# Optimization experiments

Hardware: AMD Instinct MI355X
Metric: run time of the kernel (lower is better)

Reference implementation:

```python
import math
import jax, jax.numpy as jnp
import numpy as np

FILTER_ORDER = 64
FILTER_EMB_DIM = 5
HIDDEN = 256
SHIFT = 0.05
FAST_DECAY_PCT = 0.3
SLOW_DECAY_PCT = 1.5
TARGET = 0.01


def setup_inputs() -> dict:
    key = jax.random.key(0)
    ks = jax.random.split(key, 8)
    B, C, L = 8, HIDDEN, 8192

    def lin_w(k, fan_out, fan_in):
        return jax.random.normal(k, (fan_out, fan_in), jnp.float32) / np.sqrt(fan_in).astype(np.float32)

    return {
        "x": jax.random.normal(ks[0], (B, C, L), jnp.float32),
        "W1": lin_w(ks[1], FILTER_ORDER, FILTER_EMB_DIM),
        "b1": jnp.zeros((FILTER_ORDER,), jnp.float32),
        "freq0": jnp.ones((1, FILTER_ORDER), jnp.float32),
        "W2": lin_w(ks[2], FILTER_ORDER, FILTER_ORDER),
        "b2": jnp.zeros((FILTER_ORDER,), jnp.float32),
        "freq1": jnp.ones((1, FILTER_ORDER), jnp.float32),
        "W3": lin_w(ks[3], FILTER_ORDER, FILTER_ORDER),
        "b3": jnp.zeros((FILTER_ORDER,), jnp.float32),
        "freq2": jnp.ones((1, FILTER_ORDER), jnp.float32),
        "Wout": lin_w(ks[4], HIDDEN, FILTER_ORDER),
        "D": jax.random.normal(ks[5], (HIDDEN,), jnp.float32),
        "L": L,
    }


def _pos_emb(L):
    # HyenaDnaPositionalEmbedding: z (1, L, emb_dim), t (1, L, 1)
    t = jnp.linspace(0.0, 1.0, L, dtype=jnp.float32)[None, :, None]
    t_rescaled = jnp.linspace(0.0, L - 1, L, dtype=jnp.float32)[None, :, None]
    w = 2.0 * math.pi * t_rescaled / L  # (1, L, 1)
    bands = (FILTER_EMB_DIM - 1) // 2
    f = jnp.linspace(1e-4, bands - 1, bands, dtype=jnp.float32)[None, None]  # (1, 1, bands)
    z = jnp.concatenate([t, jnp.cos(-f * w), jnp.sin(-f * w)], axis=-1)  # (1, L, emb_dim)
    return z, t


def _filter_kernel(W1, b1, freq0, W2, b2, freq1, W3, b3, freq2, Wout, L):
    z, t = _pos_emb(L)
    h = jnp.sin(freq0 * (jnp.einsum('ble,oe->blo', z, W1) + b1))
    h = jnp.sin(freq1 * (jnp.einsum('blo,po->blp', h, W2) + b2))
    h = jnp.sin(freq2 * (jnp.einsum('blo,po->blp', h, W3) + b3))
    h = jnp.einsum('blo,do->bld', h, Wout)  # (1, L, HIDDEN)
    # exponential modulation window
    max_decay = math.log(TARGET) / FAST_DECAY_PCT
    min_decay = math.log(TARGET) / SLOW_DECAY_PCT
    deltas = jnp.linspace(min_decay, max_decay, HIDDEN, dtype=jnp.float32)[None, None]
    decay = jnp.exp(-t * jnp.abs(deltas))  # (1, L, HIDDEN)
    h = h * (decay + SHIFT)
    return h[0].T  # (HIDDEN, L) channels-major kernel


def _fftconv(u, k, D):
    # y = conv(u, k) + u * D via FFT, zero-padded to 2L (linear convolution)
    L = u.shape[-1]
    fft_size = 2 * L
    k_f = jnp.fft.rfft(k.astype(jnp.float32), n=fft_size) / fft_size  # (C, fft_size//2+1)
    u_f = jnp.fft.rfft(u.astype(jnp.float32), n=fft_size)             # (B, C, fft_size//2+1)
    y = jnp.fft.irfft(u_f * k_f, n=fft_size, norm='forward')[..., :L]
    return (y + u * D[:, None]).astype(u.dtype)


def reference(x, W1, b1, freq0, W2, b2, freq1, W3, b3, freq2, Wout, D, L):
    k = _filter_kernel(W1, b1, freq0, W2, b2, freq1, W3, b3, freq2, Wout, L)
    return _fftconv(x, k, D)
```

## Files before the change

kernel.cpp:

```cpp
#include <hip/hip_runtime.h>

#define L_SEQ 8192
#define NTH 512
#define HID 256
#define PIDX(i) ((i) + ((i) >> 5))
#define LDS_SZ 8448

#define ANG16 3.83495196971410315e-4f
#define ANG8  7.66990393942820630e-4f

__device__ __forceinline__ float2 cmul(float2 a, float2 b) {
  return make_float2(a.x*b.x - a.y*b.y, a.x*b.y + a.y*b.x);
}
__device__ __forceinline__ float2 cadd(float2 a, float2 b){ return make_float2(a.x+b.x, a.y+b.y); }
__device__ __forceinline__ float2 csub(float2 a, float2 b){ return make_float2(a.x-b.x, a.y-b.y); }

__device__ __forceinline__ void bf4_fwd(float2 a0, float2 a1, float2 a2, float2 a3,
                                        float2& o0, float2& o1, float2& o2, float2& o3) {
  float2 t0 = cadd(a0,a2), t1 = csub(a0,a2), t2 = cadd(a1,a3), t3 = csub(a1,a3);
  o0 = cadd(t0,t2);
  o2 = csub(t0,t2);
  o1 = make_float2(t1.x + t3.y, t1.y - t3.x);
  o3 = make_float2(t1.x - t3.y, t1.y + t3.x);
}
__device__ __forceinline__ void bf4_inv(float2 c0, float2 c1, float2 c2, float2 c3,
                                        float2& o0, float2& o1, float2& o2, float2& o3) {
  float2 u0 = cadd(c0,c2), u2 = csub(c0,c2), u1 = cadd(c1,c3);
  float2 v3 = make_float2(c3.y - c1.y, c1.x - c3.x);
  o0 = cadd(u0,u1); o2 = csub(u0,u1); o1 = cadd(u2,v3); o3 = csub(u2,v3);
}

__device__ __constant__ const float W16C[4] = {1.0f, 0.92387953251128674f, 0.70710678118654752f, 0.38268343236508977f};
__device__ __constant__ const float W16S[4] = {0.0f, -0.38268343236508977f, -0.70710678118654752f, -0.92387953251128674f};
__device__ __constant__ const float C16[10] = {1.0f, 0.92387953251128674f, 0.70710678118654752f, 0.38268343236508977f,
                                               0.0f, -0.38268343236508977f, -0.70710678118654752f, -0.92387953251128674f,
                                               -1.0f, -0.92387953251128674f};
__device__ __constant__ const float S16[10] = {0.0f, -0.38268343236508977f, -0.70710678118654752f, -0.92387953251128674f,
                                               -1.0f, -0.92387953251128674f, -0.70710678118654752f, -0.38268343236508977f,
                                               0.0f, 0.38268343236508977f};

template<int MB>
__device__ __forceinline__ void fwd_pair(float2* __restrict__ X, int tid) {
  const int MQ = MB / 4;
  int g = tid / MQ;
  int i2 = tid - g*MQ;
  int base = g*4*MB + i2;
  float2 e[4][4];
  #pragma unroll
  for (int a = 0; a < 4; ++a)
    #pragma unroll
    for (int b = 0; b < 4; ++b)
      e[a][b] = X[PIDX(base + a*MQ + b*MB)];
  float sb, cb;
  __sincosf(-6.2831853071795864769f * (float)i2 / (float)(4*MB), &sb, &cb);
  float2 wb = make_float2(cb, sb);
  float2 f[4][4];
  #pragma unroll
  for (int a = 0; a < 4; ++a) {
    float2 wa = cmul(wb, make_float2(W16C[a], W16S[a]));
    float2 w2 = cmul(wa, wa), w3 = cmul(w2, wa);
    float2 o0,o1,o2,o3;
    bf4_fwd(e[a][0], e[a][1], e[a][2], e[a][3], o0,o1,o2,o3);
    f[a][0] = o0; f[a][1] = cmul(o1,wa); f[a][2] = cmul(o2,w2); f[a][3] = cmul(o3,w3);
  }
  float2 wp = cmul(wb,wb); wp = cmul(wp,wp);
  float2 wp2 = cmul(wp,wp), wp3 = cmul(wp2,wp);
  #pragma unroll
  for (int b = 0; b < 4; ++b) {
    float2 o0,o1,o2,o3;
    bf4_fwd(f[0][b], f[1][b], f[2][b], f[3][b], o0,o1,o2,o3);
    X[PIDX(base + 0*MQ + b*MB)] = o0;
    X[PIDX(base + 1*MQ + b*MB)] = cmul(o1,wp);
    X[PIDX(base + 2*MQ + b*MB)] = cmul(o2,wp2);
    X[PIDX(base + 3*MQ + b*MB)] = cmul(o3,wp3);
  }
}

template<int MB>
__device__ __forceinline__ void inv_pair(float2* __restrict__ X, int tid) {
  const int MQ = MB / 4;
  int g = tid / MQ;
  int i2 = tid - g*MQ;
  int base = g*4*MB + i2;
  float2 e[4][4];
  #pragma unroll
  for (int a = 0; a < 4; ++a)
    #pragma unroll
    for (int b = 0; b < 4; ++b)
      e[a][b] = X[PIDX(base + a*MQ + b*MB)];
  float sb, cb;
  __sincosf(6.2831853071795864769f * (float)i2 / (float)(4*MB), &sb, &cb);
  float2 wb = make_float2(cb, sb);
  float2 wq = cmul(wb,wb); wq = cmul(wq,wq);
  float2 wq2 = cmul(wq,wq), wq3 = cmul(wq2,wq);
  float2 f[4][4];
  #pragma unroll
  for (int b = 0; b < 4; ++b) {
    float2 c0 = e[0][b];
    float2 c1 = cmul(e[1][b], wq);
    float2 c2 = cmul(e[2][b], wq2);
    float2 c3 = cmul(e[3][b], wq3);
    float2 o0,o1,o2,o3;
    bf4_inv(c0,c1,c2,c3, o0,o1,o2,o3);
    f[0][b]=o0; f[1][b]=o1; f[2][b]=o2; f[3][b]=o3;
  }
  #pragma unroll
  for (int a = 0; a < 4; ++a) {
    float2 W1 = cmul(wb, make_float2(W16C[a], -W16S[a]));
    float2 W2 = cmul(W1,W1), W3 = cmul(W2,W1);
    float2 c0 = f[a][0];
    float2 c1 = cmul(f[a][1], W1);
    float2 c2 = cmul(f[a][2], W2);
    float2 c3 = cmul(f[a][3], W3);
    float2 o0,o1,o2,o3;
    bf4_inv(c0,c1,c2,c3, o0,o1,o2,o3);
    X[PIDX(base + a*MQ + 0*MB)] = o0;
    X[PIDX(base + a*MQ + 1*MB)] = o1;
    X[PIDX(base + a*MQ + 2*MB)] = o2;
    X[PIDX(base + a*MQ + 3*MB)] = o3;
  }
}

__device__ __forceinline__ void fwd41(float2 P[16]) {
  #pragma unroll
  for (int i = 0; i < 4; ++i) {
    float2 o0,o1,o2,o3;
    bf4_fwd(P[i], P[i+4], P[i+8], P[i+12], o0,o1,o2,o3);
    P[i]    = o0;
    P[i+4]  = cmul(o1, make_float2(C16[i],   S16[i]));
    P[i+8]  = cmul(o2, make_float2(C16[2*i], S16[2*i]));
    P[i+12] = cmul(o3, make_float2(C16[3*i], S16[3*i]));
  }
  #pragma unroll
  for (int q = 0; q < 4; ++q) {
    float2 o0,o1,o2,o3;
    bf4_fwd(P[4*q],P[4*q+1],P[4*q+2],P[4*q+3], o0,o1,o2,o3);
    P[4*q]=o0; P[4*q+1]=o1; P[4*q+2]=o2; P[4*q+3]=o3;
  }
}
__device__ __forceinline__ void inv14(float2 P[16]) {
  #pragma unroll
  for (int q = 0; q < 4; ++q) {
    float2 o0,o1,o2,o3;
    bf4_inv(P[4*q],P[4*q+1],P[4*q+2],P[4*q+3], o0,o1,o2,o3);
    P[4*q]=o0; P[4*q+1]=o1; P[4*q+2]=o2; P[4*q+3]=o3;
  }
  #pragma unroll
  for (int i = 0; i < 4; ++i) {
    float2 c0 = P[i];
    float2 c1 = cmul(P[i+4],  make_float2(C16[i],   -S16[i]));
    float2 c2 = cmul(P[i+8],  make_float2(C16[2*i], -S16[2*i]));
    float2 c3 = cmul(P[i+12], make_float2(C16[3*i], -S16[3*i]));
    float2 o0,o1,o2,o3;
    bf4_inv(c0,c1,c2,c3, o0,o1,o2,o3);
    P[i]=o0; P[i+4]=o1; P[i+8]=o2; P[i+12]=o3;
  }
}

__global__ __launch_bounds__(256) void mlp_kernel(
    const float* __restrict__ W1, const float* __restrict__ b1, const float* __restrict__ fq0,
    const float* __restrict__ W2, const float* __restrict__ b2, const float* __restrict__ fq1,
    const float* __restrict__ W3, const float* __restrict__ b3, const float* __restrict__ fq2,
    float* __restrict__ h3g) {
  __shared__ float hs[2][16][64];
  int tid = threadIdx.x;
  int lane = tid & 63, w = tid >> 6;
  int l0 = blockIdx.x * 16;

  float w1r[5];
  #pragma unroll
  for (int e = 0; e < 5; ++e) w1r[e] = W1[lane*5+e];
  float b1v = b1[lane], f0 = fq0[lane];
  #pragma unroll
  for (int r = 0; r < 4; ++r) {
    int l = l0 + w + 4*r;
    float t = (float)l * (1.0f / (float)(L_SEQ - 1));
    float ang = 6.2831853071795864769f * (float)l / (float)L_SEQ;
    float s0, c0, s1, c1;
    __sincosf(1e-4f * ang, &s0, &c0);
    __sincosf(ang, &s1, &c1);
    float acc = b1v + t*w1r[0] + c0*w1r[1] + c1*w1r[2] - s0*w1r[3] - s1*w1r[4];
    hs[0][w + 4*r][lane] = __sinf(f0 * acc);
  }
  __syncthreads();

  float wr[64];
  #pragma unroll
  for (int j = 0; j < 16; ++j) *(float4*)&wr[4*j] = *(const float4*)&W2[lane*64 + 4*j];
  float b2v = b2[lane], f1 = fq1[lane];
  #pragma unroll
  for (int r = 0; r < 4; ++r) {
    int ll = w + 4*r;
    float a0 = 0.f, a1 = 0.f, a2 = 0.f, a3 = 0.f;
    #pragma unroll
    for (int o = 0; o < 64; o += 4) {
      a0 += hs[0][ll][o+0] * wr[o+0];
      a1 += hs[0][ll][o+1] * wr[o+1];
      a2 += hs[0][ll][o+2] * wr[o+2];
      a3 += hs[0][ll][o+3] * wr[o+3];
    }
    hs[1][ll][lane] = __sinf(f1 * (b2v + ((a0+a1)+(a2+a3))));
  }
  __syncthreads();

  #pragma unroll
  for (int j = 0; j < 16; ++j) *(float4*)&wr[4*j] = *(const float4*)&W3[lane*64 + 4*j];
  float b3v = b3[lane], f2 = fq2[lane];
  #pragma unroll
  for (int r = 0; r < 4; ++r) {
    int ll = w + 4*r;
    float a0 = 0.f, a1 = 0.f, a2 = 0.f, a3 = 0.f;
    #pragma unroll
    for (int o = 0; o < 64; o += 4) {
      a0 += hs[1][ll][o+0] * wr[o+0];
      a1 += hs[1][ll][o+1] * wr[o+1];
      a2 += hs[1][ll][o+2] * wr[o+2];
      a3 += hs[1][ll][o+3] * wr[o+3];
    }
    h3g[(size_t)(l0 + ll) * 64 + lane] = __sinf(f2 * (b3v + ((a0+a1)+(a2+a3))));
  }
}

__global__ __launch_bounds__(256) void kwrite_kernel(const float* __restrict__ h3g,
                                                     const float* __restrict__ Wout,
                                                     const float* __restrict__ Dv,
                                                     float* __restrict__ kbuf) {
  __shared__ float tileh[256][65];
  int tid = threadIdx.x;
  int l0 = blockIdx.x * 256;
  int c0 = blockIdx.y * 32;
  {
    const float4* src = (const float4*)(h3g + (size_t)l0 * 64);
    #pragma unroll
    for (int q = 0; q < 16; ++q) {
      int idx = tid + 256*q;
      int row = idx >> 4, col4 = idx & 15;
      float4 v = src[idx];
      tileh[row][col4*4+0] = v.x;
      tileh[row][col4*4+1] = v.y;
      tileh[row][col4*4+2] = v.z;
      tileh[row][col4*4+3] = v.w;
    }
  }
  __syncthreads();
  float hr[64];
  #pragma unroll
  for (int o = 0; o < 64; ++o) hr[o] = tileh[tid][o];
  int l = l0 + tid;
  float t = (float)l * (1.0f / (float)(L_SEQ - 1));
  const float mind = -3.0701134573253945f;
  const float maxd = -15.350567286626972f;
  for (int jj = 0; jj < 32; ++jj) {
    int c = c0 + jj;
    float a0 = 0.f, a1 = 0.f, a2 = 0.f, a3 = 0.f;
    #pragma unroll
    for (int o = 0; o < 64; o += 4) {
      a0 += hr[o+0] * Wout[c*64+o+0];
      a1 += hr[o+1] * Wout[c*64+o+1];
      a2 += hr[o+2] * Wout[c*64+o+2];
      a3 += hr[o+3] * Wout[c*64+o+3];
    }
    float acc = (a0+a1)+(a2+a3);
    float delta = mind + (maxd - mind) * ((float)c * (1.0f/255.0f));
    float dec = __expf(-t * fabsf(delta)) + 0.05f;
    float v = acc * dec;
    if (l == 0) v += Dv[c];
    kbuf[(size_t)c * L_SEQ + l] = v;
  }
}

__global__ __launch_bounds__(NTH) void kf_kernel(const float* __restrict__ kbuf,
                                                 float2* __restrict__ Kf) {
  __shared__ float2 X[LDS_SZ];
  int c = blockIdx.x;
  int pipe = blockIdx.y;
  int tid = threadIdx.x;
  const float* kr = kbuf + (size_t)c * L_SEQ;
  const float sc = 1.0f / 16384.0f;

  #pragma unroll
  for (int r = 0; r < 2; ++r) {
    int n = 4*tid + 2048*r;
    float4 lo = *(const float4*)(kr + n);
    float4 hi = *(const float4*)(kr + n + 4096);
    #pragma unroll
    for (int j = 0; j < 4; ++j) {
      float klo = ((const float*)&lo)[j];
      float khi = ((const float*)&hi)[j];
      float2 vlo, vhi, w8;
      if (pipe == 0) {
        float sn, cn; __sincosf(-ANG8 * (float)(n+j), &sn, &cn);
        vlo = make_float2(klo, 0.f);
        vhi = make_float2(khi, 0.f);
        w8 = make_float2(cn, sn);
      } else {
        float sn, cn; __sincosf(-ANG16 * (float)(n+j), &sn, &cn);
        vlo = make_float2(klo*cn, klo*sn);
        vhi = make_float2(khi*sn, -khi*cn);
        w8 = cmul(make_float2(cn, sn), make_float2(cn, sn));
      }
      X[PIDX(n+j)]        = cadd(vlo, vhi);
      X[PIDX(n+j+4096)]   = cmul(csub(vlo, vhi), w8);
    }
  }
  __syncthreads();
  fwd_pair<1024>(X, tid); __syncthreads();
  fwd_pair<64>(X, tid);   __syncthreads();
  {
    float2 P[16];
    int base = tid*16;
    #pragma unroll
    for (int j = 0; j < 16; ++j) P[j] = X[PIDX(base+j)];
    fwd41(P);
    float2* out = Kf + (size_t)c * 16384 + pipe*8192 + base;
    #pragma unroll
    for (int j = 0; j < 16; ++j) out[j] = make_float2(P[j].x*sc, P[j].y*sc);
  }
}

template<int PIPE>
__global__ __launch_bounds__(NTH) void conv_pipe(const float* __restrict__ x,
                                                 const float2* __restrict__ Kf,
                                                 float* __restrict__ y) {
  __shared__ float2 X[LDS_SZ];
  int c = blockIdx.x;
  int p = blockIdx.y;
  int tid = threadIdx.x;
  const float* u0 = x + ((size_t)p       * HID + c) * L_SEQ;
  const float* u1 = x + ((size_t)(p + 4) * HID + c) * L_SEQ;
  const float2* K = Kf + (size_t)c * 16384 + PIPE*8192;
  float* y0 = y + ((size_t)p       * HID + c) * L_SEQ;
  float* y1 = y + ((size_t)(p + 4) * HID + c) * L_SEQ;

  #pragma unroll
  for (int r = 0; r < 2; ++r) {
    int n = 4*tid + 2048*r;
    float4 a0 = *(const float4*)(u0 + n);
    float4 a1 = *(const float4*)(u1 + n);
    float4 b0 = *(const float4*)(u0 + n + 4096);
    float4 b1 = *(const float4*)(u1 + n + 4096);
    #pragma unroll
    for (int j = 0; j < 4; ++j) {
      float2 vlo, vhi, w8;
      if (PIPE == 0) {
        float sn, cn; __sincosf(-ANG8 * (float)(n+j), &sn, &cn);
        vlo = make_float2(((const float*)&a0)[j], ((const float*)&a1)[j]);
        vhi = make_float2(((const float*)&b0)[j], ((const float*)&b1)[j]);
        w8 = make_float2(cn, sn);
      } else {
        float sn, cn; __sincosf(-ANG16 * (float)(n+j), &sn, &cn);
        float2 w16 = make_float2(cn, sn);
        vlo = cmul(make_float2(((const float*)&a0)[j], ((const float*)&a1)[j]), w16);
        vhi = cmul(make_float2(((const float*)&b0)[j], ((const float*)&b1)[j]),
                   make_float2(sn, -cn));
        w8 = cmul(w16, w16);
      }
      X[PIDX(n+j)]      = cadd(vlo, vhi);
      X[PIDX(n+j+4096)] = cmul(csub(vlo, vhi), w8);
    }
  }
  __syncthreads();
  fwd_pair<1024>(X, tid); __syncthreads();
  fwd_pair<64>(X, tid);   __syncthreads();
  {
    float2 P[16];
    int base = tid*16;
    #pragma unroll
    for (int j = 0; j < 16; ++j) P[j] = X[PIDX(base+j)];
    fwd41(P);
    #pragma unroll
    for (int j = 0; j < 16; ++j) P[j] = cmul(P[j], K[base+j]);
    inv14(P);
    #pragma unroll
    for (int j = 0; j < 16; ++j) X[PIDX(base+j)] = P[j];
  }
  __syncthreads();
  inv_pair<64>(X, tid);   __syncthreads();
  inv_pair<1024>(X, tid); __syncthreads();
  #pragma unroll
  for (int r = 0; r < 2; ++r) {
    int n = 4*tid + 2048*r;
    float4 w00, w01, w10, w11;
    #pragma unroll
    for (int j = 0; j < 4; ++j) {
      float2 P = X[PIDX(n+j)], Q = X[PIDX(n+j+4096)];
      float2 lo, hi;
      if (PIPE == 1) {
        float sn, cn; __sincosf(ANG16 * (float)(n+j), &sn, &cn);
        float2 w16b = make_float2(cn, sn);
        float2 w8b = cmul(w16b, w16b);
        float2 t = cmul(Q, w8b);
        lo = cmul(cadd(P, t), w16b);
        hi = cmul(csub(P, t), make_float2(-w16b.y, w16b.x));
      } else {
        float sn, cn; __sincosf(ANG8 * (float)(n+j), &sn, &cn);
        float2 t = cmul(Q, make_float2(cn, sn));
        lo = cadd(P, t);
        hi = csub(P, t);
      }
      ((float*)&w00)[j] = lo.x; ((float*)&w01)[j] = lo.y;
      ((float*)&w10)[j] = hi.x; ((float*)&w11)[j] = hi.y;
    }
    if (PIPE == 0) {
      float4 p00 = *(const float4*)(y0 + n);
      float4 p01 = *(const float4*)(y1 + n);
      float4 p10 = *(const float4*)(y0 + n + 4096);
      float4 p11 = *(const float4*)(y1 + n + 4096);
      w00.x += p00.x; w00.y += p00.y; w00.z += p00.z; w00.w += p00.w;
      w01.x += p01.x; w01.y += p01.y; w01.z += p01.z; w01.w += p01.w;
      w10.x += p10.x; w10.y += p10.y; w10.z += p10.z; w10.w += p10.w;
      w11.x += p11.x; w11.y += p11.y; w11.z += p11.z; w11.w += p11.w;
    }
    *(float4*)(y0 + n)        = w00;
    *(float4*)(y1 + n)        = w01;
    *(float4*)(y0 + n + 4096) = w10;
    *(float4*)(y1 + n + 4096) = w11;
  }
}

extern "C" void kernel_launch(void* const* d_in, const int* in_sizes, int n_in,
                              void* d_out, int out_size, void* d_ws, size_t ws_size,
                              hipStream_t stream) {
  const float* x    = (const float*)d_in[0];
  const float* W1   = (const float*)d_in[1];
  const float* b1   = (const float*)d_in[2];
  const float* fq0  = (const float*)d_in[3];
  const float* W2   = (const float*)d_in[4];
  const float* b2   = (const float*)d_in[5];
  const float* fq1  = (const float*)d_in[6];
  const float* W3   = (const float*)d_in[7];
  const float* b3   = (const float*)d_in[8];
  const float* fq2  = (const float*)d_in[9];
  const float* Wout = (const float*)d_in[10];
  const float* Dv   = (const float*)d_in[11];

  float*  kbuf = (float*)d_ws;
  float2* Kf   = (float2*)((char*)d_ws + (size_t)HID * L_SEQ * sizeof(float));
  float*  h3g  = (float*)((char*)d_ws + 38ull*1024*1024);
  float*  y    = (float*)d_out;

  mlp_kernel   <<<dim3(512),    256, 0, stream>>>(W1,b1,fq0,W2,b2,fq1,W3,b3,fq2,h3g);
  kwrite_kernel<<<dim3(32, 8),  256, 0, stream>>>(h3g, Wout, Dv, kbuf);
  kf_kernel    <<<dim3(256,2),  NTH, 0, stream>>>(kbuf, Kf);
  conv_pipe<1> <<<dim3(256,4),  NTH, 0, stream>>>(x, Kf, y);
  conv_pipe<0> <<<dim3(256,4),  NTH, 0, stream>>>(x, Kf, y);
}
```

Baseline: 172.6 us.

## Fuse both conv pipes into one kernel using radix-8 FFT with 1024 threads

The two conv_pipe launches (odd and even half-spectrum) become a single kernel. It loads x once, runs both FFT pipes in sequence, and stashes the first pipe's result in registers, so y no longer has to be written and read back. The FFT moves from radix-4 pairs to radix-8 stages with 1024 threads per block and a new LDS padding. Per-element sincos calls are replaced by incremental twiddle rotation. The exchange is a heavier block with more registers and more barriers, and some precision drift from the recurrent twiddles.

```diff
diff --git a/kernel.cpp b/kernel.cpp
--- a/kernel.cpp
+++ b/kernel.cpp
@@ -1,13 +1,17 @@
 #include <hip/hip_runtime.h>
 
 #define L_SEQ 8192
-#define NTH 512
 #define HID 256
-#define PIDX(i) ((i) + ((i) >> 5))
-#define LDS_SZ 8448
+#define PIDX(i) ((i) + ((i) >> 4))
+#define LDS_SZ 8704
 
 #define ANG16 3.83495196971410315e-4f
 #define ANG8  7.66990393942820630e-4f
+#define CS16 0.99999992646571789f
+#define SN16 3.83495187571395563e-4f
+#define CS8  0.99999970586287223f
+#define SN8  7.66990318742704490e-4f
+#define C707 0.70710678118654752f
 
 __device__ __forceinline__ float2 cmul(float2 a, float2 b) {
   return make_float2(a.x*b.x - a.y*b.y, a.x*b.y + a.y*b.x);
@@ -30,131 +34,106 @@
   o0 = cadd(u0,u1); o2 = csub(u0,u1); o1 = cadd(u2,v3); o3 = csub(u2,v3);
 }
 
-__device__ __constant__ const float W16C[4] = {1.0f, 0.92387953251128674f, 0.70710678118654752f, 0.38268343236508977f};
-__device__ __constant__ const float W16S[4] = {0.0f, -0.38268343236508977f, -0.70710678118654752f, -0.92387953251128674f};
-__device__ __constant__ const float C16[10] = {1.0f, 0.92387953251128674f, 0.70710678118654752f, 0.38268343236508977f,
-                                               0.0f, -0.38268343236508977f, -0.70710678118654752f, -0.92387953251128674f,
-                                               -1.0f, -0.92387953251128674f};
-__device__ __constant__ const float S16[10] = {0.0f, -0.38268343236508977f, -0.70710678118654752f, -0.92387953251128674f,
-                                               -1.0f, -0.92387953251128674f, -0.70710678118654752f, -0.38268343236508977f,
-                                               0.0f, 0.38268343236508977f};
-
-template<int MB>
-__device__ __forceinline__ void fwd_pair(float2* __restrict__ X, int tid) {
-  const int MQ = MB / 4;
-  int g = tid / MQ;
-  int i2 = tid - g*MQ;
-  int base = g*4*MB + i2;
-  float2 e[4][4];
-  #pragma unroll
-  for (int a = 0; a < 4; ++a)
-    #pragma unroll
-    for (int b = 0; b < 4; ++b)
-      e[a][b] = X[PIDX(base + a*MQ + b*MB)];
+__device__ __forceinline__ void fwd8(float2 P[8]) {
+  float2 e0=cadd(P[0],P[4]), e1=cadd(P[1],P[5]), e2=cadd(P[2],P[6]), e3=cadd(P[3],P[7]);
+  float2 o0=csub(P[0],P[4]), o1=csub(P[1],P[5]), o2=csub(P[2],P[6]), o3=csub(P[3],P[7]);
+  o1 = make_float2((o1.x+o1.y)*C707, (o1.y-o1.x)*C707);
+  o2 = make_float2(o2.y, -o2.x);
+  o3 = make_float2((o3.y-o3.x)*C707, -(o3.x+o3.y)*C707);
+  float2 q0,q1,q2,q3;
+  bf4_fwd(e0,e1,e2,e3,q0,q1,q2,q3);
+  P[0]=q0; P[2]=q1; P[4]=q2; P[6]=q3;
+  bf4_fwd(o0,o1,o2,o3,q0,q1,q2,q3);
+  P[1]=q0; P[3]=q1; P[5]=q2; P[7]=q3;
+}
+__device__ __forceinline__ void inv8(float2 P[8]) {
+  float2 E0,E1,E2,E3,O0,O1,O2,O3;
+  bf4_inv(P[0],P[2],P[4],P[6],E0,E1,E2,E3);
+  bf4_inv(P[1],P[3],P[5],P[7],O0,O1,O2,O3);
+  O1 = make_float2((O1.x-O1.y)*C707, (O1.x+O1.y)*C707);
+  O2 = make_float2(-O2.y, O2.x);
+  O3 = make_float2(-(O3.x+O3.y)*C707, (O3.x-O3.y)*C707);
+  P[0]=cadd(E0,O0); P[4]=csub(E0,O0);
+  P[1]=cadd(E1,O1); P[5]=csub(E1,O1);
+  P[2]=cadd(E2,O2); P[6]=csub(E2,O2);
+  P[3]=cadd(E3,O3); P[7]=csub(E3,O3);
+}
+
+template<int M>
+__device__ __forceinline__ void fwd_stage8(float2* __restrict__ X, int t) {
+  int i2 = t & (M-1);
+  int g  = t / M;
+  int base = g*8*M + i2;
+  float2 P[8];
+  #pragma unroll
+  for (int j=0;j<8;++j) P[j] = X[PIDX(base + j*M)];
+  fwd8(P);
   float sb, cb;
-  __sincosf(-6.2831853071795864769f * (float)i2 / (float)(4*MB), &sb, &cb);
-  float2 wb = make_float2(cb, sb);
-  float2 f[4][4];
-  #pragma unroll
-  for (int a = 0; a < 4; ++a) {
-    float2 wa = cmul(wb, make_float2(W16C[a], W16S[a]));
-    float2 w2 = cmul(wa, wa), w3 = cmul(w2, wa);
-    float2 o0,o1,o2,o3;
-    bf4_fwd(e[a][0], e[a][1], e[a][2], e[a][3], o0,o1,o2,o3);
-    f[a][0] = o0; f[a][1] = cmul(o1,wa); f[a][2] = cmul(o2,w2); f[a][3] = cmul(o3,w3);
-  }
-  float2 wp = cmul(wb,wb); wp = cmul(wp,wp);
-  float2 wp2 = cmul(wp,wp), wp3 = cmul(wp2,wp);
-  #pragma unroll
-  for (int b = 0; b < 4; ++b) {
-    float2 o0,o1,o2,o3;
-    bf4_fwd(f[0][b], f[1][b], f[2][b], f[3][b], o0,o1,o2,o3);
-    X[PIDX(base + 0*MQ + b*MB)] = o0;
-    X[PIDX(base + 1*MQ + b*MB)] = cmul(o1,wp);
-    X[PIDX(base + 2*MQ + b*MB)] = cmul(o2,wp2);
-    X[PIDX(base + 3*MQ + b*MB)] = cmul(o3,wp3);
-  }
-}
-
-template<int MB>
-__device__ __forceinline__ void inv_pair(float2* __restrict__ X, int tid) {
-  const int MQ = MB / 4;
-  int g = tid / MQ;
-  int i2 = tid - g*MQ;
-  int base = g*4*MB + i2;
-  float2 e[4][4];
-  #pragma unroll
-  for (int a = 0; a < 4; ++a)
-    #pragma unroll
-    for (int b = 0; b < 4; ++b)
-      e[a][b] = X[PIDX(base + a*MQ + b*MB)];
+  __sincosf(-6.2831853071795864769f * (float)i2 / (float)(8*M), &sb, &cb);
+  float2 w1 = make_float2(cb, sb);
+  float2 w2 = cmul(w1,w1), w3 = cmul(w2,w1), w4 = cmul(w2,w2);
+  float2 w5 = cmul(w4,w1), w6 = cmul(w4,w2), w7 = cmul(w4,w3);
+  X[PIDX(base)]     = P[0];
+  X[PIDX(base+M)]   = cmul(P[1],w1);
+  X[PIDX(base+2*M)] = cmul(P[2],w2);
+  X[PIDX(base+3*M)] = cmul(P[3],w3);
+  X[PIDX(base+4*M)] = cmul(P[4],w4);
+  X[PIDX(base+5*M)] = cmul(P[5],w5);
+  X[PIDX(base+6*M)] = cmul(P[6],w6);
+  X[PIDX(base+7*M)] = cmul(P[7],w7);
+}
+template<int M>
+__device__ __forceinline__ void inv_stage8(float2* __restrict__ X, int t) {
+  int i2 = t & (M-1);
+  int g  = t / M;
+  int base = g*8*M + i2;
   float sb, cb;
-  __sincosf(6.2831853071795864769f * (float)i2 / (float)(4*MB), &sb, &cb);
-  float2 wb = make_float2(cb, sb);
-  float2 wq = cmul(wb,wb); wq = cmul(wq,wq);
-  float2 wq2 = cmul(wq,wq), wq3 = cmul(wq2,wq);
-  float2 f[4][4];
-  #pragma unroll
-  for (int b = 0; b < 4; ++b) {
-    float2 c0 = e[0][b];
-    float2 c1 = cmul(e[1][b], wq);
-    float2 c2 = cmul(e[2][b], wq2);
-    float2 c3 = cmul(e[3][b], wq3);
-    float2 o0,o1,o2,o3;
-    bf4_inv(c0,c1,c2,c3, o0,o1,o2,o3);
-    f[0][b]=o0; f[1][b]=o1; f[2][b]=o2; f[3][b]=o3;
-  }
-  #pragma unroll
-  for (int a = 0; a < 4; ++a) {
-    float2 W1 = cmul(wb, make_float2(W16C[a], -W16S[a]));
-    float2 W2 = cmul(W1,W1), W3 = cmul(W2,W1);
-    float2 c0 = f[a][0];
-    float2 c1 = cmul(f[a][1], W1);
-    float2 c2 = cmul(f[a][2], W2);
-    float2 c3 = cmul(f[a][3], W3);
-    float2 o0,o1,o2,o3;
-    bf4_inv(c0,c1,c2,c3, o0,o1,o2,o3);
-    X[PIDX(base + a*MQ + 0*MB)] = o0;
-    X[PIDX(base + a*MQ + 1*MB)] = o1;
-    X[PIDX(base + a*MQ + 2*MB)] = o2;
-    X[PIDX(base + a*MQ + 3*MB)] = o3;
-  }
-}
-
-__device__ __forceinline__ void fwd41(float2 P[16]) {
-  #pragma unroll
-  for (int i = 0; i < 4; ++i) {
-    float2 o0,o1,o2,o3;
-    bf4_fwd(P[i], P[i+4], P[i+8], P[i+12], o0,o1,o2,o3);
-    P[i]    = o0;
-    P[i+4]  = cmul(o1, make_float2(C16[i],   S16[i]));
-    P[i+8]  = cmul(o2, make_float2(C16[2*i], S16[2*i]));
-    P[i+12] = cmul(o3, make_float2(C16[3*i], S16[3*i]));
-  }
-  #pragma unroll
-  for (int q = 0; q < 4; ++q) {
-    float2 o0,o1,o2,o3;
-    bf4_fwd(P[4*q],P[4*q+1],P[4*q+2],P[4*q+3], o0,o1,o2,o3);
-    P[4*q]=o0; P[4*q+1]=o1; P[4*q+2]=o2; P[4*q+3]=o3;
-  }
-}
-__device__ __forceinline__ void inv14(float2 P[16]) {
-  #pragma unroll
-  for (int q = 0; q < 4; ++q) {
-    float2 o0,o1,o2,o3;
-    bf4_inv(P[4*q],P[4*q+1],P[4*q+2],P[4*q+3], o0,o1,o2,o3);
-    P[4*q]=o0; P[4*q+1]=o1; P[4*q+2]=o2; P[4*q+3]=o3;
-  }
-  #pragma unroll
-  for (int i = 0; i < 4; ++i) {
-    float2 c0 = P[i];
-    float2 c1 = cmul(P[i+4],  make_float2(C16[i],   -S16[i]));
-    float2 c2 = cmul(P[i+8],  make_float2(C16[2*i], -S16[2*i]));
-    float2 c3 = cmul(P[i+12], make_float2(C16[3*i], -S16[3*i]));
-    float2 o0,o1,o2,o3;
-    bf4_inv(c0,c1,c2,c3, o0,o1,o2,o3);
-    P[i]=o0; P[i+4]=o1; P[i+8]=o2; P[i+12]=o3;
-  }
+  __sincosf(6.2831853071795864769f * (float)i2 / (float)(8*M), &sb, &cb);
+  float2 w1 = make_float2(cb, sb);
+  float2 w2 = cmul(w1,w1), w3 = cmul(w2,w1), w4 = cmul(w2,w2);
+  float2 w5 = cmul(w4,w1), w6 = cmul(w4,w2), w7 = cmul(w4,w3);
+  float2 P[8];
+  P[0] = X[PIDX(base)];
+  P[1] = cmul(X[PIDX(base+M)],  w1);
+  P[2] = cmul(X[PIDX(base+2*M)],w2);
+  P[3] = cmul(X[PIDX(base+3*M)],w3);
+  P[4] = cmul(X[PIDX(base+4*M)],w4);
+  P[5] = cmul(X[PIDX(base+5*M)],w5);
+  P[6] = cmul(X[PIDX(base+6*M)],w6);
+  P[7] = cmul(X[PIDX(base+7*M)],w7);
+  inv8(P);
+  #pragma unroll
+  for (int j=0;j<8;++j) X[PIDX(base + j*M)] = P[j];
+}
+
+__device__ __forceinline__ void fft_mid_fwd(float2* __restrict__ X, int t) {
+  __syncthreads();
+  fwd_stage8<512>(X,t); __syncthreads();
+  fwd_stage8<64>(X,t);  __syncthreads();
+  fwd_stage8<8>(X,t);   __syncthreads();
+}
+__device__ __forceinline__ void fft_mid_inv(float2* __restrict__ X, int t) {
+  __syncthreads();
+  inv_stage8<8>(X,t);   __syncthreads();
+  inv_stage8<64>(X,t);  __syncthreads();
+  inv_stage8<512>(X,t); __syncthreads();
+}
+
+__device__ __forceinline__ void middle_pointwise(float2* __restrict__ X,
+                                                 const float2* __restrict__ K, int t) {
+  int base = 8*t;
+  float2 kreg[8];
+  #pragma unroll
+  for (int r=0;r<8;++r) kreg[r] = K[base+r];
+  float2 P[8];
+  #pragma unroll
+  for (int r=0;r<8;++r) P[r] = X[PIDX(base+r)];
+  fwd8(P);
+  #pragma unroll
+  for (int r=0;r<8;++r) P[r] = cmul(P[r], kreg[r]);
+  inv8(P);
+  #pragma unroll
+  for (int r=0;r<8;++r) X[PIDX(base+r)] = P[r];
 }
 
 __global__ __launch_bounds__(256) void mlp_kernel(
@@ -269,152 +248,141 @@
   }
 }
 
-__global__ __launch_bounds__(NTH) void kf_kernel(const float* __restrict__ kbuf,
-                                                 float2* __restrict__ Kf) {
+__global__ __launch_bounds__(1024) void kf_kernel(const float* __restrict__ kbuf,
+                                                  float2* __restrict__ Kf) {
   __shared__ float2 X[LDS_SZ];
-  int c = blockIdx.x;
-  int pipe = blockIdx.y;
-  int tid = threadIdx.x;
+  int pipe = blockIdx.x;
+  int c = blockIdx.y;
+  int t = threadIdx.x;
   const float* kr = kbuf + (size_t)c * L_SEQ;
   const float sc = 1.0f / 16384.0f;
-
-  #pragma unroll
-  for (int r = 0; r < 2; ++r) {
-    int n = 4*tid + 2048*r;
-    float4 lo = *(const float4*)(kr + n);
-    float4 hi = *(const float4*)(kr + n + 4096);
-    #pragma unroll
-    for (int j = 0; j < 4; ++j) {
-      float klo = ((const float*)&lo)[j];
-      float khi = ((const float*)&hi)[j];
-      float2 vlo, vhi, w8;
-      if (pipe == 0) {
-        float sn, cn; __sincosf(-ANG8 * (float)(n+j), &sn, &cn);
-        vlo = make_float2(klo, 0.f);
-        vhi = make_float2(khi, 0.f);
-        w8 = make_float2(cn, sn);
-      } else {
-        float sn, cn; __sincosf(-ANG16 * (float)(n+j), &sn, &cn);
-        vlo = make_float2(klo*cn, klo*sn);
-        vhi = make_float2(khi*sn, -khi*cn);
-        w8 = cmul(make_float2(cn, sn), make_float2(cn, sn));
-      }
-      X[PIDX(n+j)]        = cadd(vlo, vhi);
-      X[PIDX(n+j+4096)]   = cmul(csub(vlo, vhi), w8);
-    }
-  }
-  __syncthreads();
-  fwd_pair<1024>(X, tid); __syncthreads();
-  fwd_pair<64>(X, tid);   __syncthreads();
-  {
-    float2 P[16];
-    int base = tid*16;
-    #pragma unroll
-    for (int j = 0; j < 16; ++j) P[j] = X[PIDX(base+j)];
-    fwd41(P);
-    float2* out = Kf + (size_t)c * 16384 + pipe*8192 + base;
-    #pragma unroll
-    for (int j = 0; j < 16; ++j) out[j] = make_float2(P[j].x*sc, P[j].y*sc);
-  }
-}
-
-template<int PIPE>
-__global__ __launch_bounds__(NTH) void conv_pipe(const float* __restrict__ x,
-                                                 const float2* __restrict__ Kf,
-                                                 float* __restrict__ y) {
+  int n0 = 4*t;
+  float4 lo4 = *(const float4*)(kr + n0);
+  float4 hi4 = *(const float4*)(kr + n0 + 4096);
+  if (pipe == 0) {
+    float sb, cb; __sincosf(-ANG8 * (float)n0, &sb, &cb);
+    float2 w8 = make_float2(cb, sb);
+    #pragma unroll
+    for (int j = 0; j < 4; ++j) {
+      if (j) w8 = cmul(w8, make_float2(CS8, -SN8));
+      float klo = ((const float*)&lo4)[j];
+      float khi = ((const float*)&hi4)[j];
+      X[PIDX(n0+j)]      = make_float2(klo + khi, 0.f);
+      float d = klo - khi;
+      X[PIDX(n0+j+4096)] = make_float2(d * w8.x, d * w8.y);
+    }
+  } else {
+    float sb, cb; __sincosf(-ANG16 * (float)n0, &sb, &cb);
+    float2 w16 = make_float2(cb, sb);
+    #pragma unroll
+    for (int j = 0; j < 4; ++j) {
+      if (j) w16 = cmul(w16, make_float2(CS16, -SN16));
+      float klo = ((const float*)&lo4)[j];
+      float khi = ((const float*)&hi4)[j];
+      float2 vlo = make_float2(klo * w16.x, klo * w16.y);
+      float2 vhi = make_float2(khi * w16.y, -khi * w16.x);
+      float2 w8 = cmul(w16, w16);
+      X[PIDX(n0+j)]      = cadd(vlo, vhi);
+      X[PIDX(n0+j+4096)] = cmul(csub(vlo, vhi), w8);
+    }
+  }
+  fft_mid_fwd(X, t);
+  int base = 8*t;
+  float2 P[8];
+  #pragma unroll
+  for (int r=0;r<8;++r) P[r] = X[PIDX(base+r)];
+  fwd8(P);
+  float2* out = Kf + (size_t)c * 16384 + pipe*8192 + base;
+  #pragma unroll
+  for (int r=0;r<8;++r) out[r] = make_float2(P[r].x*sc, P[r].y*sc);
+}
+
+__global__ __launch_bounds__(1024) void conv_kernel(const float* __restrict__ x,
+                                                    const float2* __restrict__ Kf,
+                                                    float* __restrict__ y) {
   __shared__ float2 X[LDS_SZ];
-  int c = blockIdx.x;
-  int p = blockIdx.y;
-  int tid = threadIdx.x;
+  int p = blockIdx.x;
+  int c = blockIdx.y;
+  int t = threadIdx.x;
   const float* u0 = x + ((size_t)p       * HID + c) * L_SEQ;
   const float* u1 = x + ((size_t)(p + 4) * HID + c) * L_SEQ;
-  const float2* K = Kf + (size_t)c * 16384 + PIPE*8192;
+  const float2* KA = Kf + (size_t)c * 16384;
+  const float2* KB = KA + 8192;
   float* y0 = y + ((size_t)p       * HID + c) * L_SEQ;
   float* y1 = y + ((size_t)(p + 4) * HID + c) * L_SEQ;
 
-  #pragma unroll
-  for (int r = 0; r < 2; ++r) {
-    int n = 4*tid + 2048*r;
-    float4 a0 = *(const float4*)(u0 + n);
-    float4 a1 = *(const float4*)(u1 + n);
-    float4 b0 = *(const float4*)(u0 + n + 4096);
-    float4 b1 = *(const float4*)(u1 + n + 4096);
-    #pragma unroll
-    for (int j = 0; j < 4; ++j) {
-      float2 vlo, vhi, w8;
-      if (PIPE == 0) {
-        float sn, cn; __sincosf(-ANG8 * (float)(n+j), &sn, &cn);
-        vlo = make_float2(((const float*)&a0)[j], ((const float*)&a1)[j]);
-        vhi = make_float2(((const float*)&b0)[j], ((const float*)&b1)[j]);
-        w8 = make_float2(cn, sn);
-      } else {
-        float sn, cn; __sincosf(-ANG16 * (float)(n+j), &sn, &cn);
-        float2 w16 = make_float2(cn, sn);
-        vlo = cmul(make_float2(((const float*)&a0)[j], ((const float*)&a1)[j]), w16);
-        vhi = cmul(make_float2(((const float*)&b0)[j], ((const float*)&b1)[j]),
-                   make_float2(sn, -cn));
-        w8 = cmul(w16, w16);
-      }
-      X[PIDX(n+j)]      = cadd(vlo, vhi);
-      X[PIDX(n+j+4096)] = cmul(csub(vlo, vhi), w8);
-    }
-  }
-  __syncthreads();
-  fwd_pair<1024>(X, tid); __syncthreads();
-  fwd_pair<64>(X, tid);   __syncthreads();
+  int n0 = 4*t;
+  float4 a0 = *(const float4*)(u0 + n0);
+  float4 a1 = *(const float4*)(u1 + n0);
+  float4 b0 = *(const float4*)(u0 + n0 + 4096);
+  float4 b1 = *(const float4*)(u1 + n0 + 4096);
+
   {
-    float2 P[16];
-    int base = tid*16;
-    #pragma unroll
-    for (int j = 0; j < 16; ++j) P[j] = X[PIDX(base+j)];
-    fwd41(P);
-    #pragma unroll
-    for (int j = 0; j < 16; ++j) P[j] = cmul(P[j], K[base+j]);
-    inv14(P);
-    #pragma unroll
-    for (int j = 0; j < 16; ++j) X[PIDX(base+j)] = P[j];
-  }
-  __syncthreads();
-  inv_pair<64>(X, tid);   __syncthreads();
-  inv_pair<1024>(X, tid); __syncthreads();
-  #pragma unroll
-  for (int r = 0; r < 2; ++r) {
-    int n = 4*tid + 2048*r;
+    float sb, cb; __sincosf(-ANG16 * (float)n0, &sb, &cb);
+    float2 w16 = make_float2(cb, sb);
+    #pragma unroll
+    for (int j = 0; j < 4; ++j) {
+      if (j) w16 = cmul(w16, make_float2(CS16, -SN16));
+      float2 vlo = cmul(make_float2(((const float*)&a0)[j], ((const float*)&a1)[j]), w16);
+      float2 vhi = cmul(make_float2(((const float*)&b0)[j], ((const float*)&b1)[j]),
+                        make_float2(w16.y, -w16.x));
+      float2 w8 = cmul(w16, w16);
+      X[PIDX(n0+j)]      = cadd(vlo, vhi);
+      X[PIDX(n0+j+4096)] = cmul(csub(vlo, vhi), w8);
+    }
+  }
+  fft_mid_fwd(X, t);
+  middle_pointwise(X, KB, t);
+  fft_mid_inv(X, t);
+  float2 stash[8];
+  {
+    float sb, cb; __sincosf(ANG16 * (float)n0, &sb, &cb);
+    float2 w16b = make_float2(cb, sb);
+    #pragma unroll
+    for (int j = 0; j < 4; ++j) {
+      if (j) w16b = cmul(w16b, make_float2(CS16, SN16));
+      float2 P = X[PIDX(n0+j)], Q = X[PIDX(n0+j+4096)];
+      float2 w8b = cmul(w16b, w16b);
+      float2 tt = cmul(Q, w8b);
+      stash[j]   = cmul(cadd(P, tt), w16b);
+      stash[4+j] = cmul(csub(P, tt), make_float2(-w16b.y, w16b.x));
+    }
+  }
+  __syncthreads();
+
+  {
+    float sb, cb; __sincosf(-ANG8 * (float)n0, &sb, &cb);
+    float2 w8 = make_float2(cb, sb);
+    #pragma unroll
+    for (int j = 0; j < 4; ++j) {
+      if (j) w8 = cmul(w8, make_float2(CS8, -SN8));
+      float2 vlo = make_float2(((const float*)&a0)[j], ((const float*)&a1)[j]);
+      float2 vhi = make_float2(((const float*)&b0)[j], ((const float*)&b1)[j]);
+      X[PIDX(n0+j)]      = cadd(vlo, vhi);
+      X[PIDX(n0+j+4096)] = cmul(csub(vlo, vhi), w8);
+    }
+  }
+  fft_mid_fwd(X, t);
+  middle_pointwise(X, KA, t);
+  fft_mid_inv(X, t);
+  {
+    float sb, cb; __sincosf(ANG8 * (float)n0, &sb, &cb);
+    float2 w8b = make_float2(cb, sb);
     float4 w00, w01, w10, w11;
     #pragma unroll
     for (int j = 0; j < 4; ++j) {
-      float2 P = X[PIDX(n+j)], Q = X[PIDX(n+j+4096)];
-      float2 lo, hi;
-      if (PIPE == 1) {
-        float sn, cn; __sincosf(ANG16 * (float)(n+j), &sn, &cn);
-        float2 w16b = make_float2(cn, sn);
-        float2 w8b = cmul(w16b, w16b);
-        float2 t = cmul(Q, w8b);
-        lo = cmul(cadd(P, t), w16b);
-        hi = cmul(csub(P, t), make_float2(-w16b.y, w16b.x));
-      } else {
-        float sn, cn; __sincosf(ANG8 * (float)(n+j), &sn, &cn);
-        float2 t = cmul(Q, make_float2(cn, sn));
-        lo = cadd(P, t);
-        hi = csub(P, t);
-      }
+      if (j) w8b = cmul(w8b, make_float2(CS8, SN8));
+      float2 P = X[PIDX(n0+j)], Q = X[PIDX(n0+j+4096)];
+      float2 tt = cmul(Q, w8b);
+      float2 lo = cadd(cadd(P, tt), stash[j]);
+      float2 hi = cadd(csub(P, tt), stash[4+j]);
       ((float*)&w00)[j] = lo.x; ((float*)&w01)[j] = lo.y;
       ((float*)&w10)[j] = hi.x; ((float*)&w11)[j] = hi.y;
     }
-    if (PIPE == 0) {
-      float4 p00 = *(const float4*)(y0 + n);
-      float4 p01 = *(const float4*)(y1 + n);
-      float4 p10 = *(const float4*)(y0 + n + 4096);
-      float4 p11 = *(const float4*)(y1 + n + 4096);
-      w00.x += p00.x; w00.y += p00.y; w00.z += p00.z; w00.w += p00.w;
-      w01.x += p01.x; w01.y += p01.y; w01.z += p01.z; w01.w += p01.w;
-      w10.x += p10.x; w10.y += p10.y; w10.z += p10.z; w10.w += p10.w;
-      w11.x += p11.x; w11.y += p11.y; w11.z += p11.z; w11.w += p11.w;
-    }
-    *(float4*)(y0 + n)        = w00;
-    *(float4*)(y1 + n)        = w01;
-    *(float4*)(y0 + n + 4096) = w10;
-    *(float4*)(y1 + n + 4096) = w11;
+    *(float4*)(y0 + n0)        = w00;
+    *(float4*)(y1 + n0)        = w01;
+    *(float4*)(y0 + n0 + 4096) = w10;
+    *(float4*)(y1 + n0 + 4096) = w11;
   }
 }
 
@@ -439,9 +407,8 @@
   float*  h3g  = (float*)((char*)d_ws + 38ull*1024*1024);
   float*  y    = (float*)d_out;
 
-  mlp_kernel   <<<dim3(512),    256, 0, stream>>>(W1,b1,fq0,W2,b2,fq1,W3,b3,fq2,h3g);
-  kwrite_kernel<<<dim3(32, 8),  256, 0, stream>>>(h3g, Wout, Dv, kbuf);
-  kf_kernel    <<<dim3(256,2),  NTH, 0, stream>>>(kbuf, Kf);
-  conv_pipe<1> <<<dim3(256,4),  NTH, 0, stream>>>(x, Kf, y);
-  conv_pipe<0> <<<dim3(256,4),  NTH, 0, stream>>>(x, Kf, y);
-}
+  mlp_kernel   <<<dim3(512),   256,  0, stream>>>(W1,b1,fq0,W2,b2,fq1,W3,b3,fq2,h3g);
+  kwrite_kernel<<<dim3(32, 8), 256,  0, stream>>>(h3g, Wout, Dv, kbuf);
+  kf_kernel    <<<dim3(2, 256), 1024, 0, stream>>>(kbuf, Kf);
+  conv_kernel  <<<dim3(4, 256), 1024, 0, stream>>>(x, Kf, y);
+}
```

Result: slower. 239.8 us (+38.9%).
